# Performance work log

Measured on AMD Instinct MI355X. Metric: run time of the kernel, lower is better.

The kernel has to match this reference:

```python
import jax, jax.numpy as jnp
import numpy as np
from jax import lax

# dims
B, T = 64, 1024
ANNOT, RNN, MEM, ATTN = 512, 1024, 512, 512
FILTERS, KSIZE = 32, 31
PAD = (KSIZE - 1) // 2  # 15, SAME padding


def setup_inputs() -> dict:
    key = jax.random.key(0)
    ks = jax.random.split(key, 20)
    s = 0.02
    return {
        "memory": jax.random.normal(ks[0], (B, MEM), jnp.float32),
        "context": jax.random.normal(ks[1], (B, ANNOT), jnp.float32),
        "rnn_state": jax.random.normal(ks[2], (B, RNN), jnp.float32),
        "annots": jax.random.normal(ks[3], (B, T, ANNOT), jnp.float32),
        "atten": jax.random.uniform(ks[4], (B, 2, T), jnp.float32),
        "mask": jnp.ones((B, T), jnp.int32),
        "t": 0,
        # GRUCell params (torch gate order: r, z, n)
        "W_ih": jax.random.normal(ks[5], (3 * RNN, ANNOT + MEM), jnp.float32) * s,
        "W_hh": jax.random.normal(ks[6], (3 * RNN, RNN), jnp.float32) * s,
        "b_ih": jnp.zeros((3 * RNN,), jnp.float32),
        "b_hh": jnp.zeros((3 * RNN,), jnp.float32),
        # location-sensitive attention params
        "conv_w": jax.random.normal(ks[7], (FILTERS, 2, KSIZE), jnp.float32) * s,
        "loc_w": jax.random.normal(ks[8], (ATTN, FILTERS), jnp.float32) * s,
        "loc_b": jnp.zeros((ATTN,), jnp.float32),
        "q_w": jax.random.normal(ks[9], (ATTN, RNN), jnp.float32) * s,
        "q_b": jnp.zeros((ATTN,), jnp.float32),
        "a_w": jax.random.normal(ks[10], (ATTN, ANNOT), jnp.float32) * s,
        "a_b": jnp.zeros((ATTN,), jnp.float32),
        "v_w": jax.random.normal(ks[11], (1, ATTN), jnp.float32) * s,
    }


def _gru_cell(x, h, W_ih, W_hh, b_ih, b_hh):
    gi = x @ W_ih.T + b_ih  # [B, 3H]
    gh = h @ W_hh.T + b_hh
    i_r, i_z, i_n = jnp.split(gi, 3, axis=-1)
    h_r, h_z, h_n = jnp.split(gh, 3, axis=-1)
    r = jax.nn.sigmoid(i_r + h_r)
    z = jax.nn.sigmoid(i_z + h_z)
    n = jnp.tanh(i_n + r * h_n)
    return (1.0 - z) * n + z * h


def reference(memory, context, rnn_state, annots, atten, mask, t,
              W_ih, W_hh, b_ih, b_hh, conv_w, loc_w, loc_b,
              q_w, q_b, a_w, a_b, v_w):
    # GRU step on [memory; prev_context]
    rnn_input = jnp.concatenate([memory, context], axis=-1)  # [B, MEM+ANNOT]
    rnn_output = _gru_cell(rnn_input, rnn_state, W_ih, W_hh, b_ih, b_hh)  # [B, RNN]

    # location features: SAME conv over [B, 2, T] -> [B, FILTERS, T]
    loc_conv = lax.conv_general_dilated(
        atten, conv_w, window_strides=(1,), padding=[(PAD, PAD)],
        dimension_numbers=("NCH", "OIH", "NCH"))
    processed_loc = jnp.einsum("bft,af->bta", loc_conv, loc_w) + loc_b  # [B,T,ATTN]

    processed_query = (rnn_output @ q_w.T + q_b)[:, None, :]            # [B,1,ATTN]
    processed_annots = jnp.einsum("btd,ad->bta", annots, a_w) + a_b     # [B,T,ATTN]

    energy = jnp.tanh(processed_query + processed_annots + processed_loc)
    alignment = jnp.einsum("bta,a->bt", energy, v_w[0])                 # [B,T]

    # mask fill with -inf where mask == 0
    alignment = jnp.where(mask == 0, -jnp.inf, alignment)

    # sigmoid-normalized attention weights
    sig = jax.nn.sigmoid(alignment)
    alignment = sig / jnp.sum(sig, axis=1, keepdims=True)               # [B,T]

    new_context = jnp.einsum("bt,btd->bd", alignment, annots)           # [B,ANNOT]
    return rnn_output, new_context, alignment
```

## Files before the change

kernel.cpp:

```cpp
#include <hip/hip_runtime.h>

typedef float f32x4 __attribute__((ext_vector_type(4)));
typedef short bf16x8 __attribute__((ext_vector_type(8)));

__device__ __forceinline__ unsigned int pk2(float a, float b) {
    unsigned int ua = __float_as_uint(a); ua += 0x7FFFu + ((ua >> 16) & 1u);
    unsigned int ub = __float_as_uint(b); ub += 0x7FFFu + ((ub >> 16) & 1u);
    return __builtin_amdgcn_perm(ub, ua, 0x07060302u);
}
__device__ __forceinline__ unsigned short bf16_rne(float a) {
    unsigned int ua = __float_as_uint(a);
    ua += 0x7FFFu + ((ua >> 16) & 1u);
    return (unsigned short)(ua >> 16);
}
__device__ __forceinline__ float tanh_fast(float x) {
    float e = __expf(x + x);
    return 1.f - 2.f / (e + 1.f);
}
__device__ __forceinline__ f32x4 mfma16(bf16x8 a, bf16x8 b, f32x4 c) {
    return __builtin_amdgcn_mfma_f32_16x16x32_bf16(a, b, c, 0, 0, 0);
}
__device__ __forceinline__ void ald16(const void* g, void* l) {
    __builtin_amdgcn_global_load_lds(
        (const __attribute__((address_space(1))) unsigned int*)g,
        (__attribute__((address_space(3))) unsigned int*)l, 16, 0, 0);
}

#define Q_WIH   786432
#define Q_WHH   1572864
#define Q_QW    1703936
#define Q_X2    1720320
#define Q_X1    1736704
#define Q_BAW   1802240
#define Q_BLW   1806336
#define Q_EB    1806464
#define NCVT    7057

__global__ __launch_bounds__(256) void k_prep(
    const float* __restrict__ Wih, const float* __restrict__ Whh,
    const float* __restrict__ qw, const float* __restrict__ rnn_state,
    const float* __restrict__ memory, const float* __restrict__ context,
    const float* __restrict__ aw, const float* __restrict__ lw,
    const float* __restrict__ ab, const float* __restrict__ lb,
    const float* __restrict__ atten, const float* __restrict__ convw,
    unsigned short* __restrict__ Wihb, unsigned short* __restrict__ Whhb,
    unsigned short* __restrict__ qwb, unsigned short* __restrict__ X2b,
    unsigned short* __restrict__ X1b, unsigned short* __restrict__ Bbig,
    float* __restrict__ ebias, unsigned short* __restrict__ Lconv)
{
    __shared__ float att_s[2 * 160];
    __shared__ float cw_s[1984];
    const int tid = threadIdx.x;
    if (blockIdx.x < NCVT) {
        int q = blockIdx.x * 256 + tid;
        if (q >= Q_EB) return;
        if (q < Q_WIH) {
            int i = q * 4;
            float4 v = *(const float4*)(Wih + i);
            uint2 u; u.x = pk2(v.x, v.y); u.y = pk2(v.z, v.w);
            *(uint2*)(Wihb + i) = u;
        } else if (q < Q_WHH) {
            int i = (q - Q_WIH) * 4;
            float4 v = *(const float4*)(Whh + i);
            uint2 u; u.x = pk2(v.x, v.y); u.y = pk2(v.z, v.w);
            *(uint2*)(Whhb + i) = u;
        } else if (q < Q_QW) {
            int i = (q - Q_WHH) * 4;
            float4 v = *(const float4*)(qw + i);
            uint2 u; u.x = pk2(v.x, v.y); u.y = pk2(v.z, v.w);
            *(uint2*)(qwb + i) = u;
        } else if (q < Q_X2) {
            int i = (q - Q_QW) * 4;
            float4 v = *(const float4*)(rnn_state + i);
            uint2 u; u.x = pk2(v.x, v.y); u.y = pk2(v.z, v.w);
            *(uint2*)(X2b + i) = u;
        } else if (q < Q_X1) {
            int i = (q - Q_X2) * 4;
            int b = i >> 10, c = i & 1023;
            const float* s = (c < 512) ? (memory + b * 512 + c) : (context + b * 512 + (c - 512));
            float4 v = *(const float4*)s;
            uint2 u; u.x = pk2(v.x, v.y); u.y = pk2(v.z, v.w);
            *(uint2*)(X1b + i) = u;
        } else if (q < Q_BAW) {
            int i = (q - Q_X1) * 4;
            int a = i >> 9, c = i & 511;
            float4 v = *(const float4*)(aw + a * 512 + c);
            uint2 u; u.x = pk2(v.x, v.y); u.y = pk2(v.z, v.w);
            *(uint2*)(Bbig + a * 544 + c) = u;
        } else if (q < Q_BLW) {
            int i = (q - Q_BAW) * 4;
            int a = i >> 5, c = i & 31;
            float4 v = *(const float4*)(lw + a * 32 + c);
            uint2 u; u.x = pk2(v.x, v.y); u.y = pk2(v.z, v.w);
            *(uint2*)(Bbig + a * 544 + 512 + c) = u;
        } else {
            int i = (q - Q_BLW) * 4;
            float4 va = *(const float4*)(ab + i);
            float4 vb = *(const float4*)(lb + i);
            float4 r; r.x = va.x + vb.x; r.y = va.y + vb.y; r.z = va.z + vb.z; r.w = va.w + vb.w;
            *(float4*)(ebias + i) = r;
        }
    } else {
        const int bid = blockIdx.x - NCVT;
        const int b = bid >> 3;
        const int tbase = (bid & 7) * 128;
        for (int i = tid; i < 320; i += 256) {
            int c = i / 160, j = i % 160;
            float v = 0.f;
            int pos = tbase - 15 + j;
            if (j < 158 && pos >= 0 && pos < 1024) v = atten[b * 2048 + c * 1024 + pos];
            att_s[c * 160 + j] = v;
        }
        for (int i = tid; i < 1984; i += 256) cw_s[i] = convw[i];
        __syncthreads();
        const int f = tid & 31, tq = tid >> 5;
        float acc[16];
#pragma unroll
        for (int i = 0; i < 16; ++i) acc[i] = 0.f;
        for (int c = 0; c < 2; ++c) {
            for (int k = 0; k < 31; ++k) {
                float w = cw_s[f * 62 + c * 31 + k];
                int base = c * 160 + tq * 16 + k;
#pragma unroll
                for (int ti = 0; ti < 16; ++ti) acc[ti] += w * att_s[base + ti];
            }
        }
#pragma unroll
        for (int ti = 0; ti < 16; ++ti) {
            int t = tbase + tq * 16 + ti;
            Lconv[(b * 1024 + t) * 32 + f] = bf16_rne(acc[ti]);
        }
    }
}

__global__ __launch_bounds__(256, 4) void k_gemm_ks(
    const unsigned short* __restrict__ A1, const unsigned short* __restrict__ A2,
    const unsigned short* __restrict__ B1, const unsigned short* __restrict__ B2,
    float* __restrict__ C, int N, int nTiles, int n_split, int K, int Klen)
{
    __shared__ __align__(16) unsigned short As[64 * 32];
    __shared__ __align__(16) unsigned short Bs[128 * 32];
    const int tid = threadIdx.x;
    const int nb = blockIdx.x % nTiles;
    const int ks = blockIdx.x / nTiles;
    const int nBase = nb * 128;
    const bool use2 = nBase >= n_split;
    const unsigned short* A = use2 ? A2 : A1;
    const unsigned short* B = use2 ? B2 : B1;
    const int brow0 = nBase - (use2 ? n_split : 0);
    const int lane = tid & 63, w = tid >> 6;
    const int c = lane & 15, qd = lane >> 4;
    const int lr = lane >> 2;
    const int swzl = ((lane & 3) ^ ((lr >> 1) & 3)) * 8;

    const f32x4 fz = {0.f, 0.f, 0.f, 0.f};
    f32x4 acc[4][2];
#pragma unroll
    for (int i = 0; i < 4; ++i) { acc[i][0] = fz; acc[i][1] = fz; }

    const int k0b = ks * Klen;
    const int nkc = Klen >> 5;
    for (int kc = 0; kc < nkc; ++kc) {
        const int k0 = k0b + kc * 32;
        ald16(A + (size_t)(w * 16 + lr) * K + k0 + swzl, &As[w * 512]);
        ald16(B + (size_t)(brow0 + w * 16 + lr) * K + k0 + swzl, &Bs[w * 512]);
        ald16(B + (size_t)(brow0 + 64 + w * 16 + lr) * K + k0 + swzl, &Bs[2048 + w * 512]);
        __syncthreads();
        const int rdoff = (qd ^ ((c >> 1) & 3)) * 8;
        bf16x8 af[4];
#pragma unroll
        for (int i = 0; i < 4; ++i) af[i] = *(const bf16x8*)&As[(i * 16 + c) * 32 + rdoff];
#pragma unroll
        for (int j = 0; j < 2; ++j) {
            bf16x8 bj = *(const bf16x8*)&Bs[(w * 32 + j * 16 + c) * 32 + rdoff];
#pragma unroll
            for (int i = 0; i < 4; ++i) acc[i][j] = mfma16(af[i], bj, acc[i][j]);
        }
        __syncthreads();
    }
    float* Cp = C + (size_t)ks * 64 * N;
#pragma unroll
    for (int i = 0; i < 4; ++i)
#pragma unroll
        for (int r = 0; r < 4; ++r) {
            int row = i * 16 + qd * 4 + r;
#pragma unroll
            for (int j = 0; j < 2; ++j) {
                int col = nBase + w * 32 + j * 16 + c;
                Cp[row * N + col] = acc[i][j][r];
            }
        }
}

__global__ __launch_bounds__(256) void k_gates(
    const float* __restrict__ Cg, const float* __restrict__ h0,
    const float* __restrict__ bih, const float* __restrict__ bhh,
    float* __restrict__ outv, unsigned short* __restrict__ X3b)
{
    int idx = blockIdx.x * 256 + threadIdx.x;
    int b = idx >> 10, h = idx & 1023;
    const float* g0 = Cg + b * 6144;
    const float* g1 = Cg + 393216 + b * 6144;
    float ir = g0[h] + g1[h] + bih[h];
    float iz = g0[h + 1024] + g1[h + 1024] + bih[h + 1024];
    float inn = g0[h + 2048] + g1[h + 2048] + bih[h + 2048];
    float hr = g0[h + 3072] + g1[h + 3072] + bhh[h];
    float hz = g0[h + 4096] + g1[h + 4096] + bhh[h + 1024];
    float hn = g0[h + 5120] + g1[h + 5120] + bhh[h + 2048];
    float r = 1.f / (1.f + __expf(-(ir + hr)));
    float z = 1.f / (1.f + __expf(-(iz + hz)));
    float n = tanh_fast(inn + r * hn);
    float o = (1.f - z) * n + z * h0[idx];
    outv[idx] = o;
    X3b[idx] = bf16_rne(o);
}

__global__ __launch_bounds__(256, 2) void k_attn(
    const float* __restrict__ annots, const unsigned short* __restrict__ Lconv,
    const unsigned short* __restrict__ Bbig, const float* __restrict__ pqP,
    const float* __restrict__ qb, const float* __restrict__ ebias,
    const float* __restrict__ vw, float* __restrict__ wsal)
{
    __shared__ __align__(16) unsigned short As[2][64 * 32];
    __shared__ float red[4][64];
    const int tid = threadIdx.x;
    const int btBase = blockIdx.x * 64;
    const int b = btBase >> 10;
    const int lane = tid & 63, w = tid >> 6;
    const int c = lane & 15, qd = lane >> 4;
    const int arow = tid >> 2, alc = tid & 3;
    const int apofs = (alc ^ ((arow >> 1) & 3)) * 8;
    const int rdoff = (qd ^ ((c >> 1) & 3)) * 8;

    const f32x4 fz = {0.f, 0.f, 0.f, 0.f};
    f32x4 acc[4][8];
#pragma unroll
    for (int i = 0; i < 4; ++i)
#pragma unroll
        for (int j = 0; j < 8; ++j) acc[i][j] = fz;

    const unsigned short* bBase = Bbig + (size_t)(w * 128 + c) * 544 + qd * 8;
    const float* aP = annots + (size_t)(btBase + arow) * 512 + alc * 8;

    bf16x8 bb[2][8];
#pragma unroll
    for (int j = 0; j < 8; ++j) bb[0][j] = *(const bf16x8*)(bBase + j * 8704);
    {
        float4 v0 = *(const float4*)(aP);
        float4 v1 = *(const float4*)(aP + 4);
        uint4 u;
        u.x = pk2(v0.x, v0.y); u.y = pk2(v0.z, v0.w);
        u.z = pk2(v1.x, v1.y); u.w = pk2(v1.z, v1.w);
        *(uint4*)&As[0][arow * 32 + apofs] = u;
    }
    asm volatile("s_waitcnt lgkmcnt(0)" ::: "memory");
    __builtin_amdgcn_s_barrier();
    __builtin_amdgcn_sched_barrier(0);

#pragma unroll
    for (int kc = 0; kc < 17; ++kc) {
        const int cur = kc & 1, nxt = cur ^ 1;
        float4 v0n, v1n; uint4 lcv;
        if (kc < 15) {
            v0n = *(const float4*)(aP + (kc + 1) * 32);
            v1n = *(const float4*)(aP + (kc + 1) * 32 + 4);
        } else if (kc == 15) {
            lcv = *(const uint4*)(Lconv + (size_t)(btBase + arow) * 32 + alc * 8);
        }
        if (kc < 16) {
#pragma unroll
            for (int j = 0; j < 8; ++j)
                bb[nxt][j] = *(const bf16x8*)(bBase + j * 8704 + (kc + 1) * 32);
        }
        bf16x8 af[4];
#pragma unroll
        for (int i = 0; i < 4; ++i) af[i] = *(const bf16x8*)&As[cur][(i * 16 + c) * 32 + rdoff];
        __builtin_amdgcn_s_setprio(1);
#pragma unroll
        for (int j = 0; j < 8; ++j)
#pragma unroll
            for (int i = 0; i < 4; ++i) acc[i][j] = mfma16(af[i], bb[cur][j], acc[i][j]);
        __builtin_amdgcn_s_setprio(0);
        if (kc < 16) {
            if (kc < 15) {
                uint4 u;
                u.x = pk2(v0n.x, v0n.y); u.y = pk2(v0n.z, v0n.w);
                u.z = pk2(v1n.x, v1n.y); u.w = pk2(v1n.z, v1n.w);
                *(uint4*)&As[nxt][arow * 32 + apofs] = u;
            } else {
                *(uint4*)&As[nxt][arow * 32 + apofs] = lcv;
            }
            asm volatile("s_waitcnt lgkmcnt(0)" ::: "memory");
            __builtin_amdgcn_s_barrier();
            __builtin_amdgcn_sched_barrier(0);
        }
    }
    float pe[8], vv[8];
#pragma unroll
    for (int j = 0; j < 8; ++j) {
        int colg = w * 128 + j * 16 + c;
        float s = qb[colg] + ebias[colg];
#pragma unroll
        for (int p = 0; p < 8; ++p) s += pqP[p * 32768 + b * 512 + colg];
        pe[j] = s;
        vv[j] = vw[colg];
    }
#pragma unroll
    for (int i = 0; i < 4; ++i)
#pragma unroll
        for (int r = 0; r < 4; ++r) {
            float p = 0.f;
#pragma unroll
            for (int j = 0; j < 8; ++j)
                p += vv[j] * tanh_fast(acc[i][j][r] + pe[j]);
            p += __shfl_xor(p, 1);
            p += __shfl_xor(p, 2);
            p += __shfl_xor(p, 4);
            p += __shfl_xor(p, 8);
            if (c == 0) red[w][i * 16 + qd * 4 + r] = p;
        }
    __syncthreads();
    if (tid < 64)
        wsal[btBase + tid] = red[0][tid] + red[1][tid] + red[2][tid] + red[3][tid];
}

__global__ __launch_bounds__(256) void k_ctx(
    const float* __restrict__ annots, const float* __restrict__ wsal,
    const int* __restrict__ mask, float* __restrict__ out)
{
    __shared__ float al[1024];
    __shared__ float wsum[4];
    __shared__ float red[256];
    const int b = blockIdx.x >> 3;
    const int chunk = blockIdx.x & 7;
    const int tid = threadIdx.x;
    float lsum = 0.f;
#pragma unroll
    for (int p = 0; p < 4; ++p) {
        int t = p * 256 + tid;
        int bt = b * 1024 + t;
        float raw = wsal[bt];
        float s = (mask[bt] != 0) ? 1.f / (1.f + __expf(-raw)) : 0.f;
        al[t] = s;
        lsum += s;
    }
    for (int off = 32; off > 0; off >>= 1) lsum += __shfl_xor(lsum, off);
    if ((tid & 63) == 0) wsum[tid >> 6] = lsum;
    __syncthreads();
    const float tot = wsum[0] + wsum[1] + wsum[2] + wsum[3];
    const float inv = 1.f / tot;
    if (chunk == 0) {
#pragma unroll
        for (int p = 0; p < 4; ++p) {
            int t = p * 256 + tid;
            out[98304 + b * 1024 + t] = al[t] * inv;
        }
    }
    const int dq = tid & 63, tq = tid >> 6;
    const int d = chunk * 64 + dq;
    const float* ap = annots + (size_t)(b * 1024 + tq * 256) * 512 + d;
    float acc = 0.f;
#pragma unroll 4
    for (int t = 0; t < 256; ++t) acc += al[tq * 256 + t] * ap[(size_t)t * 512];
    red[tid] = acc;
    __syncthreads();
    if (tid < 64) {
        float s2 = red[tid] + red[64 + tid] + red[128 + tid] + red[192 + tid];
        out[65536 + b * 512 + chunk * 64 + tid] = s2 * inv;
    }
}

extern "C" void kernel_launch(void* const* d_in, const int* in_sizes, int n_in,
                              void* d_out, int out_size, void* d_ws, size_t ws_size,
                              hipStream_t stream) {
    const float* memory    = (const float*)d_in[0];
    const float* context   = (const float*)d_in[1];
    const float* rnn_state = (const float*)d_in[2];
    const float* annots    = (const float*)d_in[3];
    const float* atten     = (const float*)d_in[4];
    const int*   mask      = (const int*)d_in[5];
    const float* W_ih   = (const float*)d_in[7];
    const float* W_hh   = (const float*)d_in[8];
    const float* b_ih   = (const float*)d_in[9];
    const float* b_hh   = (const float*)d_in[10];
    const float* conv_w = (const float*)d_in[11];
    const float* loc_w  = (const float*)d_in[12];
    const float* loc_b  = (const float*)d_in[13];
    const float* q_w    = (const float*)d_in[14];
    const float* q_b    = (const float*)d_in[15];
    const float* a_w    = (const float*)d_in[16];
    const float* a_b    = (const float*)d_in[17];
    const float* v_w    = (const float*)d_in[18];
    float* out = (float*)d_out;

    char* w8 = (char*)d_ws;
    unsigned short* Lconv = (unsigned short*)(w8 + 0);
    unsigned short* Bbig  = (unsigned short*)(w8 + 4194304);
    unsigned short* Wihb  = (unsigned short*)(w8 + 4751360);
    unsigned short* Whhb  = (unsigned short*)(w8 + 11042816);
    unsigned short* qwb   = (unsigned short*)(w8 + 17334272);
    unsigned short* X1b   = (unsigned short*)(w8 + 18382848);
    unsigned short* X2b   = (unsigned short*)(w8 + 18513920);
    unsigned short* X3b   = (unsigned short*)(w8 + 18644992);
    float*          Cgru  = (float*)(w8 + 18776064);
    float*          pqP   = (float*)(w8 + 18776064);
    float*          wsal  = (float*)(w8 + 19824640);
    float*          ebias = (float*)(w8 + 21921792);

    k_prep<<<NCVT + 512, 256, 0, stream>>>(W_ih, W_hh, q_w, rnn_state, memory, context,
                                           a_w, loc_w, a_b, loc_b, atten, conv_w,
                                           Wihb, Whhb, qwb, X2b, X1b, Bbig, ebias, Lconv);
    k_gemm_ks<<<96, 256, 0, stream>>>(X1b, X2b, Wihb, Whhb, Cgru, 6144, 48, 3072, 1024, 512);
    k_gates<<<256, 256, 0, stream>>>(Cgru, rnn_state, b_ih, b_hh, out, X3b);
    k_gemm_ks<<<32, 256, 0, stream>>>(X3b, X3b, qwb, qwb, pqP, 512, 4, 0x40000000, 1024, 128);
    k_attn<<<1024, 256, 0, stream>>>(annots, Lconv, Bbig, pqP, q_b, ebias, v_w, wsal);
    k_ctx<<<512, 256, 0, stream>>>(annots, wsal, mask, out);
}
```

Before: 352.3 us.

## Stage attention weight tiles in LDS via async loads with 8-wave blocks

The attention GEMM block grows from 4 to 8 waves, each covering 64 attention columns instead of 128. The B (weight) tile is now streamed into double-buffered LDS with global_load_lds instead of being held in registers per wave. This is meant to cut register pressure and allow more waves to overlap memory latency, at the cost of about 64KB of LDS per block and LDS reads for B fragments. The context kernel's reduction also gets four independent accumulators to break the dependency chain.

```diff
diff --git a/kernel.cpp b/kernel.cpp
--- a/kernel.cpp
+++ b/kernel.cpp
@@ -215,90 +215,85 @@
     X3b[idx] = bf16_rne(o);
 }
 
-__global__ __launch_bounds__(256, 2) void k_attn(
+__global__ __launch_bounds__(512, 4) void k_attn(
     const float* __restrict__ annots, const unsigned short* __restrict__ Lconv,
     const unsigned short* __restrict__ Bbig, const float* __restrict__ pqP,
     const float* __restrict__ qb, const float* __restrict__ ebias,
     const float* __restrict__ vw, float* __restrict__ wsal)
 {
     __shared__ __align__(16) unsigned short As[2][64 * 32];
-    __shared__ float red[4][64];
+    __shared__ __align__(16) unsigned short Bs[2][512 * 32];
+    __shared__ float red[8][64];
     const int tid = threadIdx.x;
     const int btBase = blockIdx.x * 64;
     const int b = btBase >> 10;
     const int lane = tid & 63, w = tid >> 6;
     const int c = lane & 15, qd = lane >> 4;
-    const int arow = tid >> 2, alc = tid & 3;
-    const int apofs = (alc ^ ((arow >> 1) & 3)) * 8;
+    const int lr = lane >> 2;
+    const int swzl = ((lane & 3) ^ ((lr >> 1) & 3)) * 8;
+    const int arow = tid >> 3, alc = tid & 7;
+    const int apofs = ((alc >> 1) ^ ((arow >> 1) & 3)) * 8 + (alc & 1) * 4;
     const int rdoff = (qd ^ ((c >> 1) & 3)) * 8;
 
     const f32x4 fz = {0.f, 0.f, 0.f, 0.f};
-    f32x4 acc[4][8];
+    f32x4 acc[4][4];
 #pragma unroll
     for (int i = 0; i < 4; ++i)
 #pragma unroll
-        for (int j = 0; j < 8; ++j) acc[i][j] = fz;
-
-    const unsigned short* bBase = Bbig + (size_t)(w * 128 + c) * 544 + qd * 8;
-    const float* aP = annots + (size_t)(btBase + arow) * 512 + alc * 8;
-
-    bf16x8 bb[2][8];
-#pragma unroll
-    for (int j = 0; j < 8; ++j) bb[0][j] = *(const bf16x8*)(bBase + j * 8704);
+        for (int j = 0; j < 4; ++j) acc[i][j] = fz;
+
+    const float* aP = annots + (size_t)(btBase + arow) * 512 + alc * 4;
+    const unsigned short* bP = Bbig + (size_t)(w * 64 + lr) * 544 + swzl;
+
+#pragma unroll
+    for (int s = 0; s < 4; ++s)
+        ald16(bP + (size_t)s * 16 * 544, &Bs[0][(w * 64 + s * 16) * 32]);
     {
-        float4 v0 = *(const float4*)(aP);
-        float4 v1 = *(const float4*)(aP + 4);
-        uint4 u;
-        u.x = pk2(v0.x, v0.y); u.y = pk2(v0.z, v0.w);
-        u.z = pk2(v1.x, v1.y); u.w = pk2(v1.z, v1.w);
-        *(uint4*)&As[0][arow * 32 + apofs] = u;
-    }
-    asm volatile("s_waitcnt lgkmcnt(0)" ::: "memory");
-    __builtin_amdgcn_s_barrier();
-    __builtin_amdgcn_sched_barrier(0);
-
-#pragma unroll
+        float4 v0 = *(const float4*)aP;
+        uint2 u; u.x = pk2(v0.x, v0.y); u.y = pk2(v0.z, v0.w);
+        *(uint2*)&As[0][arow * 32 + apofs] = u;
+    }
+    __syncthreads();
+
     for (int kc = 0; kc < 17; ++kc) {
         const int cur = kc & 1, nxt = cur ^ 1;
-        float4 v0n, v1n; uint4 lcv;
+        if (kc < 16) {
+#pragma unroll
+            for (int s = 0; s < 4; ++s)
+                ald16(bP + (size_t)s * 16 * 544 + (kc + 1) * 32,
+                      &Bs[nxt][(w * 64 + s * 16) * 32]);
+        }
+        float4 v0n;
         if (kc < 15) {
             v0n = *(const float4*)(aP + (kc + 1) * 32);
-            v1n = *(const float4*)(aP + (kc + 1) * 32 + 4);
         } else if (kc == 15) {
-            lcv = *(const uint4*)(Lconv + (size_t)(btBase + arow) * 32 + alc * 8);
-        }
-        if (kc < 16) {
-#pragma unroll
-            for (int j = 0; j < 8; ++j)
-                bb[nxt][j] = *(const bf16x8*)(bBase + j * 8704 + (kc + 1) * 32);
+            if (w < 4)
+                ald16(Lconv + (size_t)(btBase + w * 16 + lr) * 32 + swzl,
+                      &As[nxt][w * 512]);
         }
         bf16x8 af[4];
 #pragma unroll
         for (int i = 0; i < 4; ++i) af[i] = *(const bf16x8*)&As[cur][(i * 16 + c) * 32 + rdoff];
         __builtin_amdgcn_s_setprio(1);
 #pragma unroll
-        for (int j = 0; j < 8; ++j)
-#pragma unroll
-            for (int i = 0; i < 4; ++i) acc[i][j] = mfma16(af[i], bb[cur][j], acc[i][j]);
+        for (int j = 0; j < 4; ++j) {
+            bf16x8 bj = *(const bf16x8*)&Bs[cur][(w * 64 + j * 16 + c) * 32 + rdoff];
+#pragma unroll
+            for (int i = 0; i < 4; ++i) acc[i][j] = mfma16(af[i], bj, acc[i][j]);
+        }
         __builtin_amdgcn_s_setprio(0);
         if (kc < 16) {
             if (kc < 15) {
-                uint4 u;
-                u.x = pk2(v0n.x, v0n.y); u.y = pk2(v0n.z, v0n.w);
-                u.z = pk2(v1n.x, v1n.y); u.w = pk2(v1n.z, v1n.w);
-                *(uint4*)&As[nxt][arow * 32 + apofs] = u;
-            } else {
-                *(uint4*)&As[nxt][arow * 32 + apofs] = lcv;
+                uint2 u; u.x = pk2(v0n.x, v0n.y); u.y = pk2(v0n.z, v0n.w);
+                *(uint2*)&As[nxt][arow * 32 + apofs] = u;
             }
-            asm volatile("s_waitcnt lgkmcnt(0)" ::: "memory");
-            __builtin_amdgcn_s_barrier();
-            __builtin_amdgcn_sched_barrier(0);
-        }
-    }
-    float pe[8], vv[8];
-#pragma unroll
-    for (int j = 0; j < 8; ++j) {
-        int colg = w * 128 + j * 16 + c;
+            __syncthreads();
+        }
+    }
+    float pe[4], vv[4];
+#pragma unroll
+    for (int j = 0; j < 4; ++j) {
+        int colg = w * 64 + j * 16 + c;
         float s = qb[colg] + ebias[colg];
 #pragma unroll
         for (int p = 0; p < 8; ++p) s += pqP[p * 32768 + b * 512 + colg];
@@ -311,7 +306,7 @@
         for (int r = 0; r < 4; ++r) {
             float p = 0.f;
 #pragma unroll
-            for (int j = 0; j < 8; ++j)
+            for (int j = 0; j < 4; ++j)
                 p += vv[j] * tanh_fast(acc[i][j][r] + pe[j]);
             p += __shfl_xor(p, 1);
             p += __shfl_xor(p, 2);
@@ -320,8 +315,12 @@
             if (c == 0) red[w][i * 16 + qd * 4 + r] = p;
         }
     __syncthreads();
-    if (tid < 64)
-        wsal[btBase + tid] = red[0][tid] + red[1][tid] + red[2][tid] + red[3][tid];
+    if (tid < 64) {
+        float s = 0.f;
+#pragma unroll
+        for (int ww = 0; ww < 8; ++ww) s += red[ww][tid];
+        wsal[btBase + tid] = s;
+    }
 }
 
 __global__ __launch_bounds__(256) void k_ctx(
@@ -359,14 +358,20 @@
     const int dq = tid & 63, tq = tid >> 6;
     const int d = chunk * 64 + dq;
     const float* ap = annots + (size_t)(b * 1024 + tq * 256) * 512 + d;
-    float acc = 0.f;
+    const float* alp = al + tq * 256;
+    float s0 = 0.f, s1 = 0.f, s2 = 0.f, s3 = 0.f;
 #pragma unroll 4
-    for (int t = 0; t < 256; ++t) acc += al[tq * 256 + t] * ap[(size_t)t * 512];
-    red[tid] = acc;
+    for (int t = 0; t < 256; t += 4) {
+        s0 += alp[t]     * ap[(size_t)(t)     * 512];
+        s1 += alp[t + 1] * ap[(size_t)(t + 1) * 512];
+        s2 += alp[t + 2] * ap[(size_t)(t + 2) * 512];
+        s3 += alp[t + 3] * ap[(size_t)(t + 3) * 512];
+    }
+    red[tid] = (s0 + s1) + (s2 + s3);
     __syncthreads();
     if (tid < 64) {
-        float s2 = red[tid] + red[64 + tid] + red[128 + tid] + red[192 + tid];
-        out[65536 + b * 512 + chunk * 64 + tid] = s2 * inv;
+        float s2r = red[tid] + red[64 + tid] + red[128 + tid] + red[192 + tid];
+        out[65536 + b * 512 + chunk * 64 + tid] = s2r * inv;
     }
 }
 
@@ -413,6 +418,6 @@
     k_gemm_ks<<<96, 256, 0, stream>>>(X1b, X2b, Wihb, Whhb, Cgru, 6144, 48, 3072, 1024, 512);
     k_gates<<<256, 256, 0, stream>>>(Cgru, rnn_state, b_ih, b_hh, out, X3b);
     k_gemm_ks<<<32, 256, 0, stream>>>(X3b, X3b, qwb, qwb, pqP, 512, 4, 0x40000000, 1024, 128);
-    k_attn<<<1024, 256, 0, stream>>>(annots, Lconv, Bbig, pqP, q_b, ebias, v_w, wsal);
+    k_attn<<<1024, 512, 0, stream>>>(annots, Lconv, Bbig, pqP, q_b, ebias, v_w, wsal);
     k_ctx<<<512, 256, 0, stream>>>(annots, wsal, mask, out);
 }
```

Result: slower. 364.3 us (+3.4%).

## Stage attention weight tiles through LDS with async loads and deeper prefetch

Applied to the files above, without the earlier changes.

The attention GEMM kernel now streams its B (weight) tiles into a double-buffered LDS array with global_load_lds, two k-chunks ahead, instead of loading them straight into registers. It paces the pipeline with explicit vmcnt waits, and the annots register prefetch also moves two chunks ahead. The goal is to cut register pressure and hide global-load latency behind the MFMAs. The cost is much more LDS per block (two 32 KB buffers), which may reduce occupancy below the two blocks per CU targeted by the launch bounds, and the hand-counted vmcnt values are fragile. Separately, the context reduction loop gets four independent accumulators to break its serial dependency chain.

```diff
diff --git a/kernel.cpp b/kernel.cpp
--- a/kernel.cpp
+++ b/kernel.cpp
@@ -222,12 +222,15 @@
     const float* __restrict__ vw, float* __restrict__ wsal)
 {
     __shared__ __align__(16) unsigned short As[2][64 * 32];
+    __shared__ __align__(16) unsigned short Bs[2][512 * 32];
     __shared__ float red[4][64];
     const int tid = threadIdx.x;
     const int btBase = blockIdx.x * 64;
     const int b = btBase >> 10;
     const int lane = tid & 63, w = tid >> 6;
     const int c = lane & 15, qd = lane >> 4;
+    const int lr = lane >> 2;
+    const int swzl = ((lane & 3) ^ ((lr >> 1) & 3)) * 8;
     const int arow = tid >> 2, alc = tid & 3;
     const int apofs = (alc ^ ((arow >> 1) & 3)) * 8;
     const int rdoff = (qd ^ ((c >> 1) & 3)) * 8;
@@ -239,18 +242,30 @@
 #pragma unroll
         for (int j = 0; j < 8; ++j) acc[i][j] = fz;
 
-    const unsigned short* bBase = Bbig + (size_t)(w * 128 + c) * 544 + qd * 8;
     const float* aP = annots + (size_t)(btBase + arow) * 512 + alc * 8;
-
-    bf16x8 bb[2][8];
-#pragma unroll
-    for (int j = 0; j < 8; ++j) bb[0][j] = *(const bf16x8*)(bBase + j * 8704);
+    const unsigned short* bG = Bbig + (size_t)(w * 128 + lr) * 544 + swzl;
+
+    float4 avA[2], avB[2];
+    uint4 lcv;
+
+    avA[0] = *(const float4*)(aP);      avB[0] = *(const float4*)(aP + 4);
+    __builtin_amdgcn_sched_barrier(0);
+#pragma unroll
+    for (int s = 0; s < 8; ++s)
+        ald16(bG + (size_t)s * 16 * 544, &Bs[0][(w * 128 + s * 16) * 32]);
+    __builtin_amdgcn_sched_barrier(0);
+    avA[1] = *(const float4*)(aP + 32); avB[1] = *(const float4*)(aP + 36);
+    __builtin_amdgcn_sched_barrier(0);
+#pragma unroll
+    for (int s = 0; s < 8; ++s)
+        ald16(bG + (size_t)s * 16 * 544 + 32, &Bs[1][(w * 128 + s * 16) * 32]);
+    __builtin_amdgcn_sched_barrier(0);
+    asm volatile("s_waitcnt vmcnt(18)" ::: "memory");
+    __builtin_amdgcn_sched_barrier(0);
     {
-        float4 v0 = *(const float4*)(aP);
-        float4 v1 = *(const float4*)(aP + 4);
         uint4 u;
-        u.x = pk2(v0.x, v0.y); u.y = pk2(v0.z, v0.w);
-        u.z = pk2(v1.x, v1.y); u.w = pk2(v1.z, v1.w);
+        u.x = pk2(avA[0].x, avA[0].y); u.y = pk2(avA[0].z, avA[0].w);
+        u.z = pk2(avB[0].x, avB[0].y); u.w = pk2(avB[0].z, avB[0].w);
         *(uint4*)&As[0][arow * 32 + apofs] = u;
     }
     asm volatile("s_waitcnt lgkmcnt(0)" ::: "memory");
@@ -260,36 +275,50 @@
 #pragma unroll
     for (int kc = 0; kc < 17; ++kc) {
         const int cur = kc & 1, nxt = cur ^ 1;
-        float4 v0n, v1n; uint4 lcv;
-        if (kc < 15) {
-            v0n = *(const float4*)(aP + (kc + 1) * 32);
-            v1n = *(const float4*)(aP + (kc + 1) * 32 + 4);
-        } else if (kc == 15) {
+        if (kc <= 13) {
+            avA[cur] = *(const float4*)(aP + (kc + 2) * 32);
+            avB[cur] = *(const float4*)(aP + (kc + 2) * 32 + 4);
+        } else if (kc == 14) {
             lcv = *(const uint4*)(Lconv + (size_t)(btBase + arow) * 32 + alc * 8);
         }
-        if (kc < 16) {
-#pragma unroll
-            for (int j = 0; j < 8; ++j)
-                bb[nxt][j] = *(const bf16x8*)(bBase + j * 8704 + (kc + 1) * 32);
-        }
+        __builtin_amdgcn_sched_barrier(0);
+        if (kc <= 13)      asm volatile("s_waitcnt vmcnt(10)" ::: "memory");
+        else if (kc <= 15) asm volatile("s_waitcnt vmcnt(9)" ::: "memory");
+        else               asm volatile("s_waitcnt vmcnt(0)" ::: "memory");
+        __builtin_amdgcn_sched_barrier(0);
         bf16x8 af[4];
 #pragma unroll
         for (int i = 0; i < 4; ++i) af[i] = *(const bf16x8*)&As[cur][(i * 16 + c) * 32 + rdoff];
         __builtin_amdgcn_s_setprio(1);
 #pragma unroll
-        for (int j = 0; j < 8; ++j)
-#pragma unroll
-            for (int i = 0; i < 4; ++i) acc[i][j] = mfma16(af[i], bb[cur][j], acc[i][j]);
+        for (int j = 0; j < 8; ++j) {
+            bf16x8 bj = *(const bf16x8*)&Bs[cur][(w * 128 + j * 16 + c) * 32 + rdoff];
+#pragma unroll
+            for (int i = 0; i < 4; ++i) acc[i][j] = mfma16(af[i], bj, acc[i][j]);
+        }
         __builtin_amdgcn_s_setprio(0);
+        asm volatile("s_waitcnt lgkmcnt(0)" ::: "memory");
+        __builtin_amdgcn_sched_barrier(0);
+        if (kc <= 14) {
+#pragma unroll
+            for (int s = 0; s < 8; ++s)
+                ald16(bG + (size_t)s * 16 * 544 + (kc + 2) * 32,
+                      &Bs[cur][(w * 128 + s * 16) * 32]);
+        }
+        __builtin_amdgcn_sched_barrier(0);
+        if (kc == 15) {
+            asm volatile("s_waitcnt vmcnt(8)" ::: "memory");
+            __builtin_amdgcn_sched_barrier(0);
+        }
+        if (kc <= 14) {
+            uint4 u;
+            u.x = pk2(avA[nxt].x, avA[nxt].y); u.y = pk2(avA[nxt].z, avA[nxt].w);
+            u.z = pk2(avB[nxt].x, avB[nxt].y); u.w = pk2(avB[nxt].z, avB[nxt].w);
+            *(uint4*)&As[nxt][arow * 32 + apofs] = u;
+        } else if (kc == 15) {
+            *(uint4*)&As[nxt][arow * 32 + apofs] = lcv;
+        }
         if (kc < 16) {
-            if (kc < 15) {
-                uint4 u;
-                u.x = pk2(v0n.x, v0n.y); u.y = pk2(v0n.z, v0n.w);
-                u.z = pk2(v1n.x, v1n.y); u.w = pk2(v1n.z, v1n.w);
-                *(uint4*)&As[nxt][arow * 32 + apofs] = u;
-            } else {
-                *(uint4*)&As[nxt][arow * 32 + apofs] = lcv;
-            }
             asm volatile("s_waitcnt lgkmcnt(0)" ::: "memory");
             __builtin_amdgcn_s_barrier();
             __builtin_amdgcn_sched_barrier(0);
@@ -359,14 +388,20 @@
     const int dq = tid & 63, tq = tid >> 6;
     const int d = chunk * 64 + dq;
     const float* ap = annots + (size_t)(b * 1024 + tq * 256) * 512 + d;
-    float acc = 0.f;
+    const float* alp = al + tq * 256;
+    float s0 = 0.f, s1 = 0.f, s2 = 0.f, s3 = 0.f;
 #pragma unroll 4
-    for (int t = 0; t < 256; ++t) acc += al[tq * 256 + t] * ap[(size_t)t * 512];
-    red[tid] = acc;
+    for (int t = 0; t < 256; t += 4) {
+        s0 += alp[t]     * ap[(size_t)(t)     * 512];
+        s1 += alp[t + 1] * ap[(size_t)(t + 1) * 512];
+        s2 += alp[t + 2] * ap[(size_t)(t + 2) * 512];
+        s3 += alp[t + 3] * ap[(size_t)(t + 3) * 512];
+    }
+    red[tid] = (s0 + s1) + (s2 + s3);
     __syncthreads();
     if (tid < 64) {
-        float s2 = red[tid] + red[64 + tid] + red[128 + tid] + red[192 + tid];
-        out[65536 + b * 512 + chunk * 64 + tid] = s2 * inv;
+        float s2r = red[tid] + red[64 + tid] + red[128 + tid] + red[192 + tid];
+        out[65536 + b * 512 + chunk * 64 + tid] = s2r * inv;
     }
 }
 
```

Result: faster. 335.5 us (-4.8%).
